# Kernel optimization log

Hardware: AMD Instinct MI355X
Metric: run time of the kernel (lower is better)

## Reference

```python
import jax, jax.numpy as jnp
import numpy as np

B, HH, WW, C = 16, 56, 56, 384
HEADS, WS, SHIFT, HID = 12, 7, 3, 1536
N = WS * WS
EPS = 1e-5


def _rel_pos_index(ws):
    coords = np.stack(np.meshgrid(np.arange(ws), np.arange(ws), indexing='ij'))  # (2, ws, ws)
    cf = coords.reshape(2, -1)
    rel = (cf[:, :, None] - cf[:, None, :]).transpose(1, 2, 0).copy()  # (N, N, 2)
    rel[:, :, 0] += ws - 1
    rel[:, :, 1] += ws - 1
    rel[:, :, 0] *= 2 * ws - 1
    return rel.sum(-1)  # (N, N) int


def _attn_mask(H, W, ws, shift):
    img = np.zeros((H, W))
    sl = (slice(0, -ws), slice(-ws, -shift), slice(-shift, None))
    cnt = 0
    for h in sl:
        for w in sl:
            img[h, w] = cnt
            cnt += 1
    mw = img.reshape(H // ws, ws, W // ws, ws).transpose(0, 2, 1, 3).reshape(-1, ws * ws)  # (nW, N)
    am = mw[:, None, :] - mw[:, :, None]
    return np.where(am != 0, -100.0, 0.0).astype(np.float32)  # (nW, N, N)

REL_IDX = jnp.asarray(_rel_pos_index(WS))
ATTN_MASK = jnp.asarray(_attn_mask(HH, WW, WS, SHIFT))


def _ln(x, w, b):
    m = x.mean(-1, keepdims=True)
    v = ((x - m) ** 2).mean(-1, keepdims=True)
    return (x - m) * jax.lax.rsqrt(v + EPS) * w + b


def _win_part(x, ws):
    b, h, w, c = x.shape
    x = x.reshape(b, h // ws, ws, w // ws, ws, c).transpose(0, 1, 3, 2, 4, 5)
    return x.reshape(-1, ws * ws, c)


def _win_rev(wins, ws, h, w):
    c = wins.shape[-1]
    b = wins.shape[0] // ((h // ws) * (w // ws))
    x = wins.reshape(b, h // ws, w // ws, ws, ws, c).transpose(0, 1, 3, 2, 4, 5)
    return x.reshape(b, h, w, c)


def setup_inputs() -> dict:
    key = jax.random.key(0)
    ks = jax.random.split(key, 12)
    s = lambda fan: 1.0 / np.sqrt(fan)
    return {
        'x': jax.random.normal(ks[0], (B, HH * WW, C), jnp.float32),
        'norm1_w': jnp.ones((C,), jnp.float32),
        'norm1_b': jnp.zeros((C,), jnp.float32),
        'qkv_w': jax.random.normal(ks[1], (3 * C, C), jnp.float32) * s(C),
        'qkv_b': jnp.zeros((3 * C,), jnp.float32),
        'bias_table': jax.random.normal(ks[2], ((2 * WS - 1) ** 2, HEADS), jnp.float32) * 0.02,
        'proj_w': jax.random.normal(ks[3], (C, C), jnp.float32) * s(C),
        'proj_b': jnp.zeros((C,), jnp.float32),
        'norm2_w': jnp.ones((C,), jnp.float32),
        'norm2_b': jnp.zeros((C,), jnp.float32),
        'mlp_w1': jax.random.normal(ks[4], (HID, C), jnp.float32) * s(C),
        'mlp_b1': jnp.zeros((HID,), jnp.float32),
        'mlp_w2': jax.random.normal(ks[5], (C, HID), jnp.float32) * s(HID),
        'mlp_b2': jnp.zeros((C,), jnp.float32),
        'H': HH,
        'W': WW,
    }


def reference(x, norm1_w, norm1_b, qkv_w, qkv_b, bias_table, proj_w, proj_b,
              norm2_w, norm2_b, mlp_w1, mlp_b1, mlp_w2, mlp_b2, H, W):
    b = x.shape[0]
    shortcut = x
    h = _ln(x, norm1_w, norm1_b).reshape(b, H, W, C)
    # cyclic shift (H, W divisible by WS -> no padding needed)
    h = jnp.roll(h, shift=(-SHIFT, -SHIFT), axis=(1, 2))
    xw = _win_part(h, WS)  # (b*nW, N, C)
    Bw = xw.shape[0]
    hd = C // HEADS
    qkv = xw @ qkv_w.T + qkv_b  # (Bw, N, 3C)
    qkv = qkv.reshape(Bw, N, 3, HEADS, hd).transpose(2, 0, 3, 1, 4)
    q, k, v = qkv[0], qkv[1], qkv[2]  # (Bw, heads, N, hd)
    attn = jnp.einsum('bhnd,bhmd->bhnm', q * (hd ** -0.5), k)
    rel_bias = bias_table[REL_IDX.reshape(-1)].reshape(N, N, HEADS).transpose(2, 0, 1)
    attn = attn + rel_bias[None]
    nW = ATTN_MASK.shape[0]
    attn = attn.reshape(Bw // nW, nW, HEADS, N, N) + ATTN_MASK[None, :, None]
    attn = jax.nn.softmax(attn.reshape(Bw, HEADS, N, N), axis=-1)
    out = jnp.einsum('bhnm,bhmd->bhnd', attn, v).transpose(0, 2, 1, 3).reshape(Bw, N, C)
    out = out @ proj_w.T + proj_b
    h = _win_rev(out, WS, H, W)
    h = jnp.roll(h, shift=(SHIFT, SHIFT), axis=(1, 2)).reshape(b, H * W, C)
    x = shortcut + h
    y = _ln(x, norm2_w, norm2_b)
    y = jax.nn.gelu(y @ mlp_w1.T + mlp_b1, approximate=False) @ mlp_w2.T + mlp_b2
    return x + y
```

## Files before the change

kernel.cpp:

```cpp
#include <hip/hip_runtime.h>

typedef unsigned short ushort_t;
typedef __attribute__((ext_vector_type(8))) short bf16x8;
typedef __attribute__((ext_vector_type(4))) float f32x4;

__device__ __forceinline__ float b2f(ushort_t u) {
    union { float f; unsigned int u32; } x; x.u32 = ((unsigned int)u) << 16; return x.f;
}
__device__ __forceinline__ ushort_t f2b(float f) {
    union { float f; unsigned int u; } x; x.f = f;
    unsigned int r = x.u + 0x7fffu + ((x.u >> 16) & 1u);
    return (ushort_t)(r >> 16);
}
__device__ __forceinline__ float ldin(const void* p, size_t i, int fp32) {
    return fp32 ? ((const float*)p)[i] : b2f(((const ushort_t*)p)[i]);
}
__device__ __forceinline__ void gl_lds16(const ushort_t* g, ushort_t* l) {
    __builtin_amdgcn_global_load_lds((const __attribute__((address_space(1))) unsigned int*)g,
                                     (__attribute__((address_space(3))) unsigned int*)l, 16, 0, 0);
}

struct Cv { const void* s; ushort_t* d; int n; };
struct CvA { Cv a[13]; };
__global__ void convert_all(CvA c, int total) {
    int fp32 = (*(const unsigned int*)c.a[0].s == 0x3F800000u);
    for (int idx = blockIdx.x * blockDim.x + threadIdx.x; idx < total; idx += gridDim.x * blockDim.x) {
        int i = idx, k = 0;
        while (k < 12 && i >= c.a[k].n) { i -= c.a[k].n; ++k; }
        c.a[k].d[i] = fp32 ? f2b(((const float*)c.a[k].s)[i]) : ((const ushort_t*)c.a[k].s)[i];
    }
}

__global__ __launch_bounds__(64) void ln_kernel(const void* __restrict__ x,
                                                const ushort_t* __restrict__ w,
                                                const ushort_t* __restrict__ bvec,
                                                ushort_t* __restrict__ out, int mode, int row_base,
                                                const void* __restrict__ flagsrc)
{
    int lr = blockIdx.x;
    int r = row_base + lr;
    int lane = threadIdx.x;
    int f32 = (mode == 1) ? 1 : (*(const unsigned int*)flagsrc == 0x3F800000u);
    long src;
    if (mode == 0) {
        int win = r / 49, pos = r % 49;
        int b = win >> 6, wy = (win >> 3) & 7, wx = win & 7;
        int py = pos / 7, px = pos - py * 7;
        int ys = wy * 7 + py + 3; if (ys >= 56) ys -= 56;
        int xs = wx * 7 + px + 3; if (xs >= 56) xs -= 56;
        src = (long)b * 3136 + ys * 56 + xs;
    } else {
        src = r;
    }
    float v[6];
    float s = 0.f, sq = 0.f;
#pragma unroll
    for (int j = 0; j < 6; ++j) {
        v[j] = ldin(x, src * 384 + lane + 64 * j, f32);
        s += v[j]; sq += v[j] * v[j];
    }
#pragma unroll
    for (int off = 32; off; off >>= 1) { s += __shfl_xor(s, off); sq += __shfl_xor(sq, off); }
    float mean = s * (1.f / 384.f);
    float var  = sq * (1.f / 384.f) - mean * mean;
    float rstd = rsqrtf(var + 1e-5f);
    ushort_t* op = out + (size_t)lr * 384;
#pragma unroll
    for (int j = 0; j < 6; ++j) {
        int c = lane + 64 * j;
        op[c] = f2b((v[j] - mean) * rstd * b2f(w[c]) + b2f(bvec[c]));
    }
}

__global__ __launch_bounds__(256) void attn_mfma(const ushort_t* __restrict__ qkv,
                                                 const ushort_t* __restrict__ bt,
                                                 ushort_t* __restrict__ out)
{
    __shared__ __align__(16) ushort_t Pb[4][64 * 72];
    __shared__ __align__(16) ushort_t Vb[4][32 * 72];
    int win = blockIdx.x;
    int t = threadIdx.x;
    int wave = t >> 6, lane = t & 63;
    int quad = lane >> 4, l16 = lane & 15;
    ushort_t* P  = Pb[wave];
    ushort_t* VT = Vb[wave];
    int wimg = win & 63;
    int wy = wimg >> 3, wx = wimg & 7;
    const float scale = 0.17677669529663687f;

    int rjv[4], cjv[4], gjv[4], cvalid[4];
#pragma unroll
    for (int jt = 0; jt < 4; ++jt) {
        int c = jt * 16 + l16;
        cvalid[jt] = (c < 49);
        int rj = c / 7, cj = c - rj * 7;
        rjv[jt] = rj; cjv[jt] = cj;
        int gjy = (wy == 7) ? (rj < 4 ? 1 : 2) : 0;
        int gjx = (wx == 7) ? (cj < 4 ? 1 : 2) : 0;
        gjv[jt] = gjy * 3 + gjx;
    }

    for (int hh = 0; hh < 3; ++hh) {
        int head = wave * 3 + hh;
        size_t base = (size_t)win * 49 * 1152 + (size_t)head * 32;

        bf16x8 qf[4], kf[4];
#pragma unroll
        for (int i = 0; i < 4; ++i) {
            int row = i * 16 + l16;
            bf16x8 z = {};
            qf[i] = z; kf[i] = z;
            if (row < 49) {
                qf[i] = *(const bf16x8*)(qkv + base + (size_t)row * 1152 + quad * 8);
                kf[i] = *(const bf16x8*)(qkv + base + (size_t)row * 1152 + 384 + quad * 8);
            }
        }
#pragma unroll
        for (int e = 0; e < 4; ++e) {
            int j = e * 16 + (lane >> 2);
            int db = (lane & 3) * 8;
            ushort_t buf[8] = {};
            if (j < 49) *(uint4*)buf = *(const uint4*)(qkv + base + (size_t)j * 1152 + 768 + db);
#pragma unroll
            for (int s = 0; s < 8; ++s) VT[(db + s) * 72 + j] = buf[s];
        }

        f32x4 Sv[4][4];
#pragma unroll
        for (int i = 0; i < 4; ++i)
#pragma unroll
            for (int j = 0; j < 4; ++j) {
                f32x4 z = {};
                Sv[i][j] = __builtin_amdgcn_mfma_f32_16x16x32_bf16(qf[i], kf[j], z, 0, 0, 0);
            }

#pragma unroll
        for (int it = 0; it < 4; ++it) {
#pragma unroll
            for (int r = 0; r < 4; ++r) {
                int m = it * 16 + quad * 4 + r;
                int ri = m / 7, ci = m - ri * 7;
                int giy = (wy == 7) ? (ri < 4 ? 1 : 2) : 0;
                int gix = (wx == 7) ? (ci < 4 ? 1 : 2) : 0;
                int gi = giy * 3 + gix;
                float vals[4];
                float vmax = -1e30f;
#pragma unroll
                for (int jt = 0; jt < 4; ++jt) {
                    float sv = -1e30f;
                    if (m < 49 && cvalid[jt]) {
                        int rel = (ri - rjv[jt] + 6) * 13 + (ci - cjv[jt] + 6);
                        sv = Sv[it][jt][r] * scale + b2f(bt[rel * 12 + head]);
                        if (gi != gjv[jt]) sv -= 100.f;
                    }
                    vals[jt] = sv;
                    vmax = fmaxf(vmax, sv);
                }
#pragma unroll
                for (int off = 1; off < 16; off <<= 1) vmax = fmaxf(vmax, __shfl_xor(vmax, off));
                float ssum = 0.f;
#pragma unroll
                for (int jt = 0; jt < 4; ++jt) { float e = expf(vals[jt] - vmax); vals[jt] = e; ssum += e; }
#pragma unroll
                for (int off = 1; off < 16; off <<= 1) ssum += __shfl_xor(ssum, off);
                float inv = 1.f / ssum;
#pragma unroll
                for (int jt = 0; jt < 4; ++jt) P[m * 72 + jt * 16 + l16] = f2b(vals[jt] * inv);
            }
        }

        f32x4 Ov[4][2] = {};
#pragma unroll
        for (int kk = 0; kk < 2; ++kk) {
            bf16x8 vb[2];
            vb[0] = *(const bf16x8*)&VT[(l16) * 72 + kk * 32 + quad * 8];
            vb[1] = *(const bf16x8*)&VT[(16 + l16) * 72 + kk * 32 + quad * 8];
#pragma unroll
            for (int mt = 0; mt < 4; ++mt) {
                bf16x8 pa = *(const bf16x8*)&P[(mt * 16 + l16) * 72 + kk * 32 + quad * 8];
                Ov[mt][0] = __builtin_amdgcn_mfma_f32_16x16x32_bf16(pa, vb[0], Ov[mt][0], 0, 0, 0);
                Ov[mt][1] = __builtin_amdgcn_mfma_f32_16x16x32_bf16(pa, vb[1], Ov[mt][1], 0, 0, 0);
            }
        }
#pragma unroll
        for (int mt = 0; mt < 4; ++mt)
#pragma unroll
            for (int r = 0; r < 4; ++r) {
                int m = mt * 16 + quad * 4 + r;
                if (m < 49) {
                    size_t orow = ((size_t)win * 49 + m) * 384 + (size_t)head * 32;
                    out[orow + l16]      = f2b(Ov[mt][0][r]);
                    out[orow + 16 + l16] = f2b(Ov[mt][1][r]);
                }
            }
    }
}

template <int EPI>
__global__ __launch_bounds__(256) void gemm_k(const ushort_t* __restrict__ A,
                                              const ushort_t* __restrict__ Bw,
                                              const ushort_t* __restrict__ bias,
                                              const void* __restrict__ residv,
                                              void* __restrict__ outv,
                                              int N, int K, long rbase,
                                              const void* __restrict__ flagsrc)
{
    __shared__ __align__(16) ushort_t lA[128 * 32];
    __shared__ __align__(16) ushort_t lB[128 * 32];
    int m0 = blockIdx.y * 128, n0 = blockIdx.x * 128;
    int t = threadIdx.x;
    int wave = t >> 6, lane = t & 63;
    int quad = lane >> 4, l16 = lane & 15;
    int wrow = (wave >> 1) * 64, wcol = (wave & 1) * 64;
    f32x4 acc[4][4] = {};

    int srow = wave * 32 + (lane >> 2);
    int scol = (lane & 3) * 8;
    const ushort_t* gA0 = A  + (size_t)(m0 + srow) * K + scol;
    const ushort_t* gA1 = gA0 + (size_t)16 * K;
    const ushort_t* gB0 = Bw + (size_t)(n0 + srow) * K + scol;
    const ushort_t* gB1 = gB0 + (size_t)16 * K;
    ushort_t* lA0 = &lA[wave * 1024];
    ushort_t* lA1 = &lA[wave * 1024 + 512];
    ushort_t* lB0 = &lB[wave * 1024];
    ushort_t* lB1 = &lB[wave * 1024 + 512];

    for (int k0 = 0; k0 < K; k0 += 32) {
        __syncthreads();
        gl_lds16(gA0 + k0, lA0);
        gl_lds16(gA1 + k0, lA1);
        gl_lds16(gB0 + k0, lB0);
        gl_lds16(gB1 + k0, lB1);
        __syncthreads();
        bf16x8 af[4], bf[4];
#pragma unroll
        for (int i = 0; i < 4; ++i)
            af[i] = *(const bf16x8*)(&lA[(wrow + i * 16 + l16) * 32 + quad * 8]);
#pragma unroll
        for (int j = 0; j < 4; ++j)
            bf[j] = *(const bf16x8*)(&lB[(wcol + j * 16 + l16) * 32 + quad * 8]);
#pragma unroll
        for (int i = 0; i < 4; ++i)
#pragma unroll
            for (int j = 0; j < 4; ++j)
                acc[i][j] = __builtin_amdgcn_mfma_f32_16x16x32_bf16(af[i], bf[j], acc[i][j], 0, 0, 0);
    }

    float bb[4];
#pragma unroll
    for (int j = 0; j < 4; ++j) bb[j] = b2f(bias[n0 + wcol + j * 16 + l16]);
    int rf32 = (EPI == 2) ? (*(const unsigned int*)flagsrc == 0x3F800000u) : 1;

#pragma unroll
    for (int i = 0; i < 4; ++i) {
#pragma unroll
        for (int rix = 0; rix < 4; ++rix) {
            int m = m0 + wrow + i * 16 + quad * 4 + rix;
            long orow = 0;
            if (EPI == 2) {
                long mg = rbase + m;
                int win = (int)(mg / 49), pos = (int)(mg - (long)win * 49);
                int b = win >> 6, wy = (win >> 3) & 7, wx = win & 7;
                int py = pos / 7, px = pos - py * 7;
                int y = wy * 7 + py + 3; if (y >= 56) y -= 56;
                int x = wx * 7 + px + 3; if (x >= 56) x -= 56;
                orow = (long)b * 3136 + y * 56 + x;
            } else if (EPI == 3) {
                orow = rbase + m;
            }
#pragma unroll
            for (int j = 0; j < 4; ++j) {
                int n = n0 + wcol + j * 16 + l16;
                float vv = acc[i][j][rix] + bb[j];
                if (EPI == 0) {
                    ((ushort_t*)outv)[(size_t)m * N + n] = f2b(vv);
                } else if (EPI == 1) {
                    float g = 0.5f * vv * (1.f + erff(vv * 0.70710678118f));
                    ((ushort_t*)outv)[(size_t)m * N + n] = f2b(g);
                } else {
                    float r = ldin(residv, (size_t)orow * 384 + n, rf32);
                    ((float*)outv)[(size_t)orow * 384 + n] = vv + r;
                }
            }
        }
    }
}

extern "C" void kernel_launch(void* const* d_in, const int* in_sizes, int n_in,
                              void* d_out, int out_size, void* d_ws, size_t ws_size,
                              hipStream_t stream)
{
    (void)in_sizes; (void)n_in; (void)out_size;
    char* ws = (char*)d_ws;
    size_t off = 0;
    auto alloc = [&](size_t bytes) { size_t p = off; off = (off + bytes + 255) & ~(size_t)255; return p; };

    size_t o_n1w  = alloc(384 * 2);
    size_t o_n1b  = alloc(384 * 2);
    size_t o_qw   = alloc(442368ull * 2);
    size_t o_qb   = alloc(1152 * 2);
    size_t o_bt   = alloc(2028 * 2);
    size_t o_pw   = alloc(147456ull * 2);
    size_t o_pb   = alloc(384 * 2);
    size_t o_n2w  = alloc(384 * 2);
    size_t o_n2b  = alloc(384 * 2);
    size_t o_w1   = alloc(589824ull * 2);
    size_t o_b1   = alloc(1536 * 2);
    size_t o_w2   = alloc(589824ull * 2);
    size_t o_b2   = alloc(384 * 2);

    size_t avail = (ws_size > off) ? ws_size - off : 0;
    int M_c;
    if      (avail >= (size_t)50176 * 3840 + 1024) M_c = 50176;
    else if (avail >= (size_t)12544 * 3840 + 1024) M_c = 12544;
    else                                            M_c = 6272;
    int nch = 50176 / M_c;
    size_t o_s1 = alloc((size_t)M_c * 768);
    size_t o_s2 = alloc((size_t)M_c * 3072);

    ushort_t* n1w  = (ushort_t*)(ws + o_n1w);
    ushort_t* n1b  = (ushort_t*)(ws + o_n1b);
    ushort_t* qw   = (ushort_t*)(ws + o_qw);
    ushort_t* qb   = (ushort_t*)(ws + o_qb);
    ushort_t* bt   = (ushort_t*)(ws + o_bt);
    ushort_t* pw   = (ushort_t*)(ws + o_pw);
    ushort_t* pb   = (ushort_t*)(ws + o_pb);
    ushort_t* n2w  = (ushort_t*)(ws + o_n2w);
    ushort_t* n2b  = (ushort_t*)(ws + o_n2b);
    ushort_t* w1   = (ushort_t*)(ws + o_w1);
    ushort_t* b1   = (ushort_t*)(ws + o_b1);
    ushort_t* w2   = (ushort_t*)(ws + o_w2);
    ushort_t* b2v  = (ushort_t*)(ws + o_b2);
    ushort_t* s1   = (ushort_t*)(ws + o_s1);
    ushort_t* s2   = (ushort_t*)(ws + o_s2);
    const void* x  = d_in[0];
    const void* fs = d_in[1];
    float* xmid    = (float*)d_out;

    CvA ca;
    ca.a[0]  = {d_in[1],  n1w, 384};
    ca.a[1]  = {d_in[2],  n1b, 384};
    ca.a[2]  = {d_in[3],  qw,  442368};
    ca.a[3]  = {d_in[4],  qb,  1152};
    ca.a[4]  = {d_in[5],  bt,  2028};
    ca.a[5]  = {d_in[6],  pw,  147456};
    ca.a[6]  = {d_in[7],  pb,  384};
    ca.a[7]  = {d_in[8],  n2w, 384};
    ca.a[8]  = {d_in[9],  n2b, 384};
    ca.a[9]  = {d_in[10], w1,  589824};
    ca.a[10] = {d_in[11], b1,  1536};
    ca.a[11] = {d_in[12], w2,  589824};
    ca.a[12] = {d_in[13], b2v, 384};
    convert_all<<<2048, 256, 0, stream>>>(ca, 1776492);

    for (int c = 0; c < nch; ++c) {
        int rb = c * M_c;
        ln_kernel<<<dim3(M_c), dim3(64), 0, stream>>>(x, n1w, n1b, s1, 0, rb, fs);
        gemm_k<0><<<dim3(9, M_c / 128), dim3(256), 0, stream>>>(s1, qw, qb, nullptr, s2, 1152, 384, 0, fs);
        attn_mfma<<<dim3(M_c / 49), dim3(256), 0, stream>>>(s2, bt, s1);
        gemm_k<2><<<dim3(3, M_c / 128), dim3(256), 0, stream>>>(s1, pw, pb, x, xmid, 384, 384, rb, fs);
    }
    for (int c = 0; c < nch; ++c) {
        int rb = c * M_c;
        ln_kernel<<<dim3(M_c), dim3(64), 0, stream>>>(xmid, n2w, n2b, s1, 1, rb, fs);
        gemm_k<1><<<dim3(12, M_c / 128), dim3(256), 0, stream>>>(s1, w1, b1, nullptr, s2, 1536, 384, 0, fs);
        gemm_k<3><<<dim3(3, M_c / 128), dim3(256), 0, stream>>>(s2, w2, b2v, xmid, (float*)d_out, 384, 1536, rb, fs);
    }
}
```

Measured before the change: 702.5 us.

## Enlarge GEMM block tile to 256x128 with 128x64 per-wave tiles

The GEMM kernel's block tile grows from 128x128 to 256x128 rows, so each wave now computes a 128x64 sub-tile with 32 MFMA accumulators. Each B fragment loaded from LDS is reused across twice as many A rows, and the global-to-LDS load pattern is reorganised to match. The aim is more MFMA work per LDS read and per barrier. The cost is higher register pressure (128 accumulator floats per lane), lower occupancy, and half as many blocks per launch. The smallest chunk-size option is dropped so M_c stays divisible by 256.

```diff
diff --git a/kernel.cpp b/kernel.cpp
--- a/kernel.cpp
+++ b/kernel.cpp
@@ -205,42 +205,38 @@
                                               int N, int K, long rbase,
                                               const void* __restrict__ flagsrc)
 {
-    __shared__ __align__(16) ushort_t lA[128 * 32];
+    __shared__ __align__(16) ushort_t lA[256 * 32];
     __shared__ __align__(16) ushort_t lB[128 * 32];
-    int m0 = blockIdx.y * 128, n0 = blockIdx.x * 128;
+    int m0 = blockIdx.y * 256, n0 = blockIdx.x * 128;
     int t = threadIdx.x;
     int wave = t >> 6, lane = t & 63;
     int quad = lane >> 4, l16 = lane & 15;
-    int wrow = (wave >> 1) * 64, wcol = (wave & 1) * 64;
-    f32x4 acc[4][4] = {};
-
-    int srow = wave * 32 + (lane >> 2);
+    int wr = (wave >> 1) * 128, wc = (wave & 1) * 64;
+    f32x4 acc[8][4] = {};
+
+    int sr = lane >> 2;
     int scol = (lane & 3) * 8;
-    const ushort_t* gA0 = A  + (size_t)(m0 + srow) * K + scol;
-    const ushort_t* gA1 = gA0 + (size_t)16 * K;
-    const ushort_t* gB0 = Bw + (size_t)(n0 + srow) * K + scol;
-    const ushort_t* gB1 = gB0 + (size_t)16 * K;
-    ushort_t* lA0 = &lA[wave * 1024];
-    ushort_t* lA1 = &lA[wave * 1024 + 512];
-    ushort_t* lB0 = &lB[wave * 1024];
-    ushort_t* lB1 = &lB[wave * 1024 + 512];
+    const ushort_t* gA = A  + (size_t)(m0 + wave * 64 + sr) * K + scol;
+    const ushort_t* gB = Bw + (size_t)(n0 + wave * 32 + sr) * K + scol;
+    ushort_t* lAw = &lA[wave * 64 * 32];
+    ushort_t* lBw = &lB[wave * 32 * 32];
 
     for (int k0 = 0; k0 < K; k0 += 32) {
         __syncthreads();
-        gl_lds16(gA0 + k0, lA0);
-        gl_lds16(gA1 + k0, lA1);
-        gl_lds16(gB0 + k0, lB0);
-        gl_lds16(gB1 + k0, lB1);
+#pragma unroll
+        for (int j = 0; j < 4; ++j) gl_lds16(gA + (size_t)(j * 16) * K + k0, lAw + j * 512);
+#pragma unroll
+        for (int j = 0; j < 2; ++j) gl_lds16(gB + (size_t)(j * 16) * K + k0, lBw + j * 512);
         __syncthreads();
-        bf16x8 af[4], bf[4];
-#pragma unroll
-        for (int i = 0; i < 4; ++i)
-            af[i] = *(const bf16x8*)(&lA[(wrow + i * 16 + l16) * 32 + quad * 8]);
+        bf16x8 af[8], bf[4];
+#pragma unroll
+        for (int i = 0; i < 8; ++i)
+            af[i] = *(const bf16x8*)(&lA[(wr + i * 16 + l16) * 32 + quad * 8]);
 #pragma unroll
         for (int j = 0; j < 4; ++j)
-            bf[j] = *(const bf16x8*)(&lB[(wcol + j * 16 + l16) * 32 + quad * 8]);
-#pragma unroll
-        for (int i = 0; i < 4; ++i)
+            bf[j] = *(const bf16x8*)(&lB[(wc + j * 16 + l16) * 32 + quad * 8]);
+#pragma unroll
+        for (int i = 0; i < 8; ++i)
 #pragma unroll
             for (int j = 0; j < 4; ++j)
                 acc[i][j] = __builtin_amdgcn_mfma_f32_16x16x32_bf16(af[i], bf[j], acc[i][j], 0, 0, 0);
@@ -248,14 +244,14 @@
 
     float bb[4];
 #pragma unroll
-    for (int j = 0; j < 4; ++j) bb[j] = b2f(bias[n0 + wcol + j * 16 + l16]);
+    for (int j = 0; j < 4; ++j) bb[j] = b2f(bias[n0 + wc + j * 16 + l16]);
     int rf32 = (EPI == 2) ? (*(const unsigned int*)flagsrc == 0x3F800000u) : 1;
 
 #pragma unroll
-    for (int i = 0; i < 4; ++i) {
+    for (int i = 0; i < 8; ++i) {
 #pragma unroll
         for (int rix = 0; rix < 4; ++rix) {
-            int m = m0 + wrow + i * 16 + quad * 4 + rix;
+            int m = m0 + wr + i * 16 + quad * 4 + rix;
             long orow = 0;
             if (EPI == 2) {
                 long mg = rbase + m;
@@ -270,7 +266,7 @@
             }
 #pragma unroll
             for (int j = 0; j < 4; ++j) {
-                int n = n0 + wcol + j * 16 + l16;
+                int n = n0 + wc + j * 16 + l16;
                 float vv = acc[i][j][rix] + bb[j];
                 if (EPI == 0) {
                     ((ushort_t*)outv)[(size_t)m * N + n] = f2b(vv);
@@ -310,10 +306,7 @@
     size_t o_b2   = alloc(384 * 2);
 
     size_t avail = (ws_size > off) ? ws_size - off : 0;
-    int M_c;
-    if      (avail >= (size_t)50176 * 3840 + 1024) M_c = 50176;
-    else if (avail >= (size_t)12544 * 3840 + 1024) M_c = 12544;
-    else                                            M_c = 6272;
+    int M_c = (avail >= (size_t)50176 * 3840 + 1024) ? 50176 : 12544;
     int nch = 50176 / M_c;
     size_t o_s1 = alloc((size_t)M_c * 768);
     size_t o_s2 = alloc((size_t)M_c * 3072);
@@ -356,14 +349,14 @@
     for (int c = 0; c < nch; ++c) {
         int rb = c * M_c;
         ln_kernel<<<dim3(M_c), dim3(64), 0, stream>>>(x, n1w, n1b, s1, 0, rb, fs);
-        gemm_k<0><<<dim3(9, M_c / 128), dim3(256), 0, stream>>>(s1, qw, qb, nullptr, s2, 1152, 384, 0, fs);
+        gemm_k<0><<<dim3(9, M_c / 256), dim3(256), 0, stream>>>(s1, qw, qb, nullptr, s2, 1152, 384, 0, fs);
         attn_mfma<<<dim3(M_c / 49), dim3(256), 0, stream>>>(s2, bt, s1);
-        gemm_k<2><<<dim3(3, M_c / 128), dim3(256), 0, stream>>>(s1, pw, pb, x, xmid, 384, 384, rb, fs);
+        gemm_k<2><<<dim3(3, M_c / 256), dim3(256), 0, stream>>>(s1, pw, pb, x, xmid, 384, 384, rb, fs);
     }
     for (int c = 0; c < nch; ++c) {
         int rb = c * M_c;
         ln_kernel<<<dim3(M_c), dim3(64), 0, stream>>>(xmid, n2w, n2b, s1, 1, rb, fs);
-        gemm_k<1><<<dim3(12, M_c / 128), dim3(256), 0, stream>>>(s1, w1, b1, nullptr, s2, 1536, 384, 0, fs);
-        gemm_k<3><<<dim3(3, M_c / 128), dim3(256), 0, stream>>>(s2, w2, b2v, xmid, (float*)d_out, 384, 1536, rb, fs);
-    }
-}
+        gemm_k<1><<<dim3(12, M_c / 256), dim3(256), 0, stream>>>(s1, w1, b1, nullptr, s2, 1536, 384, 0, fs);
+        gemm_k<3><<<dim3(3, M_c / 256), dim3(256), 0, stream>>>(s2, w2, b2v, xmid, (float*)d_out, 384, 1536, rb, fs);
+    }
+}
```

New measurement: 1.297 ms. 84.6% more time.
